# Kernel optimization log

Measured on AMD Instinct MI355X. Metric: run time of the kernel, lower is better.

The kernel has to match this reference:

```python
import jax, jax.numpy as jnp
import numpy as np

N_TOKENS, D_MODEL, D_HIDDEN, TOPK = 4096, 1024, 16384, 64


def setup_inputs() -> dict:
    key = jax.random.key(0)
    k0, k1, k2 = jax.random.split(key, 3)
    x = jax.random.normal(k0, (N_TOKENS, D_MODEL), dtype=jnp.float32)
    # kaiming_uniform_(a=sqrt(5)) -> bound = 1/sqrt(fan_in)
    lim_enc = 1.0 / np.sqrt(D_MODEL)
    W_enc = jax.random.uniform(k1, (D_MODEL, D_HIDDEN), jnp.float32, -lim_enc, lim_enc)
    b_enc = jnp.zeros((D_HIDDEN,), jnp.float32)
    lim_dec = 1.0 / np.sqrt(D_HIDDEN)
    W_dec = jax.random.uniform(k2, (D_HIDDEN, D_MODEL), jnp.float32, -lim_dec, lim_dec)
    # normalize_decoder=True: rows (one per feature) are unit-normalized in-place
    # under no_grad in torch, so we pre-normalize the parameter here.
    W_dec = W_dec / jnp.clip(jnp.linalg.norm(W_dec, axis=1, keepdims=True), 1e-8, None)
    b_dec = jnp.zeros((D_MODEL,), jnp.float32)
    return {"x": x, "W_enc": W_enc, "b_enc": b_enc, "W_dec": W_dec, "b_dec": b_dec, "k": TOPK}


def reference(x, W_enc, b_enc, W_dec, b_dec, k):
    # encode
    pre = x @ W_enc + b_enc                     # [N, d_hidden]
    # ReLU activation (config in ('relu','topk'))
    z = jax.nn.relu(pre)
    # TopK on |z| along feature dim, scatter original values back
    _, idx = jax.lax.top_k(jnp.abs(z), k)        # [N, k]
    rows = jnp.arange(z.shape[0])[:, None]       # [N, 1]
    z_sparse = jnp.zeros_like(z).at[rows, idx].set(jnp.take_along_axis(z, idx, axis=-1))
    # decode (W_dec rows are already unit-norm; torch re-normalizes under no_grad)
    y = z_sparse @ W_dec + b_dec                # [N, d_model]
    return y
```

## Files before the change

kernel.cpp:

```cpp
#include <hip/hip_runtime.h>

typedef unsigned short ushort_t;
typedef unsigned short ushort8 __attribute__((ext_vector_type(8)));
typedef __bf16 bf16x8 __attribute__((ext_vector_type(8)));
typedef float f32x4 __attribute__((ext_vector_type(4)));

#define N_TOKENS 4096
#define D_MODEL  1024
#define D_HIDDEN 16384
#define TOPK     64
#define DELTA    0.03f
#define RCAP     128
#define T0SEL    1.25f
#define CAP      512

__device__ __forceinline__ float bf2f(ushort_t u) {
  union { unsigned u; float f; } c; c.u = ((unsigned)u) << 16; return c.f;
}
__device__ __forceinline__ ushort_t f2bf(float f) {
  union { float f; unsigned u; } c; c.f = f;
  unsigned x = c.u;
  unsigned r = (x + 0x7FFFu + ((x >> 16) & 1u)) >> 16;
  return (ushort_t)r;
}

typedef __attribute__((address_space(1))) void GV;
typedef __attribute__((address_space(3))) void LV;
__device__ __forceinline__ void llds16(const void* g, void* l) {
  __builtin_amdgcn_global_load_lds((GV*)g, (LV*)l, 16, 0, 0);
}

__global__ __launch_bounds__(256) void cast_x_kernel(
    const float* __restrict__ in, ushort_t* __restrict__ out) {
  const int i = (blockIdx.x * 256 + threadIdx.x) * 4;
  float4 v = *(const float4*)&in[i];
  ushort4 o;
  o.x = f2bf(v.x); o.y = f2bf(v.y); o.z = f2bf(v.z); o.w = f2bf(v.w);
  *(ushort4*)&out[i] = o;
}

__global__ __launch_bounds__(256) void cast_wdec_kernel(
    const float* __restrict__ in, ushort_t* __restrict__ out) {
  const int i = (blockIdx.x * 256 + threadIdx.x) * 8;
  float4 v0 = *(const float4*)&in[i];
  float4 v1 = *(const float4*)&in[i + 4];
  ushort8 o;
  o[0] = f2bf(v0.x); o[1] = f2bf(v0.y); o[2] = f2bf(v0.z); o[3] = f2bf(v0.w);
  o[4] = f2bf(v1.x); o[5] = f2bf(v1.y); o[6] = f2bf(v1.z); o[7] = f2bf(v1.w);
  *(ushort8*)&out[i] = o;
}

__global__ __launch_bounds__(256) void transpose_cast_kernel(
    const float* __restrict__ in, ushort_t* __restrict__ outb,
    float* __restrict__ out32) {
  __shared__ float tile[64][68];
  const int tid = threadIdx.x;
  const int n0 = blockIdx.x * 64;
  const int k0 = blockIdx.y * 64;
#pragma unroll
  for (int i = 0; i < 4; ++i) {
    int e = i * 256 + tid;
    int kk = e >> 4;
    int nn = (e & 15) * 4;
    float4 v = *(const float4*)&in[(size_t)(k0 + kk) * D_HIDDEN + n0 + nn];
    tile[kk][nn + 0] = v.x;
    tile[kk][nn + 1] = v.y;
    tile[kk][nn + 2] = v.z;
    tile[kk][nn + 3] = v.w;
  }
  __syncthreads();
#pragma unroll
  for (int i = 0; i < 4; ++i) {
    int e = i * 256 + tid;
    int nn = e >> 4;
    int kk = (e & 15) * 4;
    float4 f;
    f.x = tile[kk + 0][nn];
    f.y = tile[kk + 1][nn];
    f.z = tile[kk + 2][nn];
    f.w = tile[kk + 3][nn];
    *(float4*)&out32[(size_t)(n0 + nn) * D_MODEL + k0 + kk] = f;
    ushort4 b;
    b.x = f2bf(f.x); b.y = f2bf(f.y); b.z = f2bf(f.z); b.w = f2bf(f.w);
    *(ushort4*)&outb[(size_t)(n0 + nn) * D_MODEL + k0 + kk] = b;
  }
}

__global__ __launch_bounds__(256) void encode_gemm(
    const ushort_t* __restrict__ X, const ushort_t* __restrict__ WT,
    const float* __restrict__ benc, ushort_t* __restrict__ Z) {
  __shared__ ushort_t As[128 * 32];
  __shared__ ushort_t Bs[128 * 32];
  const int tid  = threadIdx.x;
  const int wave = tid >> 6, lane = tid & 63;
  const int m0 = blockIdx.y * 128;
  const int n0 = blockIdx.x * 128;
  const int wm = (wave >> 1) * 64;
  const int wn = (wave & 1) * 64;
  const int lr = lane >> 2;
  const int lk = (lane & 3) * 8;

  f32x4 acc[4][4];
#pragma unroll
  for (int i = 0; i < 4; ++i)
#pragma unroll
    for (int j = 0; j < 4; ++j) acc[i][j] = (f32x4){0.f, 0.f, 0.f, 0.f};

  for (int k0 = 0; k0 < D_MODEL; k0 += 32) {
    __syncthreads();
#pragma unroll
    for (int c = 0; c < 2; ++c) {
      const int chunk = c * 4 + wave;
      const int m = chunk * 16 + lr;
      llds16(&X [(size_t)(m0 + m) * D_MODEL + k0 + lk], &As[chunk * 512]);
      llds16(&WT[(size_t)(n0 + m) * D_MODEL + k0 + lk], &Bs[chunk * 512]);
    }
    __syncthreads();
    bf16x8 af[4], bfr[4];
#pragma unroll
    for (int t = 0; t < 4; ++t) {
      af[t]  = *(const bf16x8*)&As[(wm + t * 16 + (lane & 15)) * 32 + (lane >> 4) * 8];
      bfr[t] = *(const bf16x8*)&Bs[(wn + t * 16 + (lane & 15)) * 32 + (lane >> 4) * 8];
    }
#pragma unroll
    for (int mt = 0; mt < 4; ++mt)
#pragma unroll
      for (int nt = 0; nt < 4; ++nt)
        acc[mt][nt] = __builtin_amdgcn_mfma_f32_16x16x32_bf16(
            af[mt], bfr[nt], acc[mt][nt], 0, 0, 0);
  }

  const int col_base = n0 + wn + (lane & 15);
  const int row_base = m0 + wm + (lane >> 4) * 4;
#pragma unroll
  for (int nt = 0; nt < 4; ++nt) {
    const float bias = benc[col_base + nt * 16];
#pragma unroll
    for (int mt = 0; mt < 4; ++mt) {
#pragma unroll
      for (int r = 0; r < 4; ++r) {
        float v = fmaxf(acc[mt][nt][r] + bias, 0.0f);
        Z[(size_t)(row_base + mt * 16 + r) * D_HIDDEN + col_base + nt * 16] = f2bf(v);
      }
    }
  }
}

__global__ __launch_bounds__(256) void topk_fused_kernel(
    const ushort_t* __restrict__ Z, const float* __restrict__ x32,
    const float* __restrict__ WT32, const float* __restrict__ benc,
    float* __restrict__ vals, int* __restrict__ idxs, int* __restrict__ flags) {
  __shared__ float  sval[CAP];
  __shared__ int    sidx[CAP];
  __shared__ int    wsum[4];
  __shared__ int    ridx[RCAP];
  __shared__ double rex[RCAP];
  __shared__ float  sV64;
  __shared__ int    selCount, refCount;
  const int tid  = threadIdx.x;
  const int lane = tid & 63;
  const int wv   = tid >> 6;
  const int row  = blockIdx.x;
  const ushort_t* zr = Z + (size_t)row * D_HIDDEN;

  ushort8 u8v[8];
#pragma unroll
  for (int i = 0; i < 8; ++i) u8v[i] = *(const ushort8*)&zr[i * 2048 + tid * 8];

  if (tid == 0) { selCount = 0; refCount = 0; }

  int cntT = 0;
#pragma unroll
  for (int i = 0; i < 8; ++i)
#pragma unroll
    for (int j = 0; j < 8; ++j) cntT += (bf2f(u8v[i][j]) > T0SEL) ? 1 : 0;

  int inc = cntT;
#pragma unroll
  for (int off = 1; off < 64; off <<= 1) {
    int y = __shfl_up(inc, off, 64);
    if (lane >= off) inc += y;
  }
  const int excT = inc - cntT;
  if (lane == 63) wsum[wv] = inc;
  __syncthreads();
  int base = excT;
  if (wv > 0) base += wsum[0];
  if (wv > 1) base += wsum[1];
  if (wv > 2) base += wsum[2];
  const int n = wsum[0] + wsum[1] + wsum[2] + wsum[3];

  int p = base;
#pragma unroll
  for (int i = 0; i < 8; ++i)
#pragma unroll
    for (int j = 0; j < 8; ++j) {
      const float f = bf2f(u8v[i][j]);
      if (f > T0SEL) {
        if (p < CAP) { sval[p] = f; sidx[p] = i * 2048 + tid * 8 + j; }
        ++p;
      }
    }
  __syncthreads();
  if (n < TOPK || n > CAP) { if (tid == 0) flags[row] = 1; return; }

  for (int j = tid; j < n; j += 256) {
    float vj = sval[j]; int ij = sidx[j];
    int rank = 0;
    for (int j2 = 0; j2 < n; ++j2) {
      float v2 = sval[j2];
      rank += (v2 > vj) || (v2 == vj && sidx[j2] < ij);
    }
    if (rank == TOPK - 1) sV64 = vj;
  }
  __syncthreads();
  const float v64 = sV64;
  if (v64 <= T0SEL + DELTA) { if (tid == 0) flags[row] = 1; return; }

  for (int j = tid; j < n; j += 256) {
    float v = sval[j];
    if (v > v64 + DELTA) {
      int p2 = atomicAdd(&selCount, 1);
      vals[(size_t)row * TOPK + p2] = v;
      idxs[(size_t)row * TOPK + p2] = sidx[j];
    } else if (v >= v64 - DELTA) {
      int c = atomicAdd(&refCount, 1);
      if (c < RCAP) ridx[c] = sidx[j];
    }
  }
  __syncthreads();
  if (refCount > RCAP) { if (tid == 0) flags[row] = 1; return; }
  if (tid == 0) flags[row] = 0;
  const int nS = selCount;
  const int nR = refCount;
  const int rNeed = TOPK - nS;

  float xr[16];
  {
    const float* xrb = &x32[(size_t)row * D_MODEL + lane * 16];
#pragma unroll
    for (int q = 0; q < 4; ++q)
      *(float4*)&xr[q * 4] = *(const float4*)&xrb[q * 4];
  }
  for (int c = wv; c < nR; c += 4) {
    const int j = ridx[c];
    const float* wr = &WT32[(size_t)j * D_MODEL];
    double p0 = 0.0, p1 = 0.0;
#pragma unroll
    for (int q = 0; q < 2; ++q) {
      const float4 wa = *(const float4*)&wr[lane * 16 + q * 8];
      const float4 wb = *(const float4*)&wr[lane * 16 + q * 8 + 4];
      p0 += (double)xr[q * 8 + 0] * wa.x + (double)xr[q * 8 + 1] * wa.y
          + (double)xr[q * 8 + 2] * wa.z + (double)xr[q * 8 + 3] * wa.w;
      p1 += (double)xr[q * 8 + 4] * wb.x + (double)xr[q * 8 + 5] * wb.y
          + (double)xr[q * 8 + 6] * wb.z + (double)xr[q * 8 + 7] * wb.w;
    }
    double part = p0 + p1;
#pragma unroll
    for (int off = 32; off > 0; off >>= 1) part += __shfl_down(part, off, 64);
    if (lane == 0) {
      double d = part + (double)benc[j];
      rex[c] = d > 0.0 ? d : 0.0;
    }
  }
  __syncthreads();

  for (int c = tid; c < nR; c += 256) {
    double vc = rex[c]; int ic = ridx[c];
    int rank = 0;
    for (int c2 = 0; c2 < nR; ++c2) {
      double v2 = rex[c2];
      rank += (v2 > vc) || (v2 == vc && ridx[c2] < ic);
    }
    if (rank < rNeed) {
      int p2 = atomicAdd(&selCount, 1);
      vals[(size_t)row * TOPK + p2] = (float)vc;
      idxs[(size_t)row * TOPK + p2] = ic;
    }
  }
}

__global__ __launch_bounds__(256) void topk_fallback_kernel(
    const int* __restrict__ flags,
    const ushort_t* __restrict__ Z, const float* __restrict__ x32,
    const float* __restrict__ WT32, const float* __restrict__ benc,
    float* __restrict__ vals, int* __restrict__ idxs) {
  if (flags[blockIdx.x] == 0) return;
  __shared__ int hist[512 * 9 + 32];
  float*  cval = (float*)hist;
  int*    cidx = (int*)hist + 512;
  int*    ridx = (int*)hist + 1024;
  double* rex  = (double*)((int*)hist + 1156);
  __shared__ int   wtot[4];
  __shared__ int   sTbin, sAbove, selCount, candCount, refCount;
  __shared__ float sV64;

  const int tid  = threadIdx.x;
  const int wave = tid >> 6, lane = tid & 63;
  const int row  = blockIdx.x;
  const ushort_t* zr = Z + (size_t)row * D_HIDDEN;

  ushort8 u8v[8];
#pragma unroll
  for (int i = 0; i < 8; ++i) u8v[i] = *(const ushort8*)&zr[i * 2048 + tid * 8];
#define ZIDX(i, j) ((i) * 2048 + tid * 8 + (j))

  for (int k = tid; k < 512 * 9; k += 256) hist[k] = 0;
  if (tid == 0) { sTbin = -1; selCount = 0; candCount = 0; refCount = 0; }
  __syncthreads();

  const int cpy = lane & 7;
#pragma unroll
  for (int i = 0; i < 8; ++i)
#pragma unroll
    for (int j = 0; j < 8; ++j) {
      ushort_t w = u8v[i][j];
      if (w) atomicAdd(&hist[((int)(w >> 6)) * 9 + cpy], 1);
    }
  __syncthreads();

  int h0 = 0, h1 = 0;
#pragma unroll
  for (int c = 0; c < 8; ++c) {
    int cc = (tid + c) & 7;
    h0 += hist[(2 * tid) * 9 + cc];
    h1 += hist[(2 * tid + 1) * 9 + cc];
  }
  const int s = h0 + h1;
  int x = s;
#pragma unroll
  for (int off = 1; off < 64; off <<= 1) {
    int y = __shfl_down(x, off, 64);
    if (lane + off < 64) x += y;
  }
  if (lane == 0) wtot[wave] = x;
  __syncthreads();
  int cross = 0;
  if (wave < 3) cross += wtot[3];
  if (wave < 2) cross += wtot[2];
  if (wave < 1) cross += wtot[1];
  const int Sexc = cross + x - s;
  if (Sexc < TOPK && Sexc + h1 >= TOPK) { sTbin = 2 * tid + 1; sAbove = Sexc; }
  const int c0 = Sexc + h1;
  if (c0 < TOPK && c0 + h0 >= TOPK) { sTbin = 2 * tid; sAbove = c0; }
  __syncthreads();
  const int Tbin = sTbin, nAbove = sAbove;

  if (Tbin < 0) {
#pragma unroll
    for (int i = 0; i < 8; ++i)
#pragma unroll
      for (int j = 0; j < 8; ++j) {
        ushort_t w = u8v[i][j];
        if (w) {
          int p = atomicAdd(&selCount, 1);
          if (p < TOPK) { vals[row * 64 + p] = bf2f(w); idxs[row * 64 + p] = ZIDX(i, j); }
        }
      }
    __syncthreads();
    for (int p2 = min(selCount, TOPK) + tid; p2 < TOPK; p2 += 256) {
      vals[row * 64 + p2] = 0.0f; idxs[row * 64 + p2] = 0;
    }
    return;
  }

#pragma unroll
  for (int i = 0; i < 8; ++i)
#pragma unroll
    for (int j = 0; j < 8; ++j) {
      ushort_t w = u8v[i][j];
      if (w && (int)(w >> 6) == Tbin) {
        int c = atomicAdd(&candCount, 1);
        if (c < 512) { cval[c] = bf2f(w); cidx[c] = ZIDX(i, j); }
      }
    }
  __syncthreads();
  {
    const int r  = TOPK - nAbove;
    const int nc = min(candCount, 512);
    for (int j = tid; j < nc; j += 256) {
      float vj = cval[j]; int ij = cidx[j];
      int rank = 0;
      for (int j2 = 0; j2 < nc; ++j2) {
        float v2 = cval[j2];
        rank += (v2 > vj) || (v2 == vj && cidx[j2] < ij);
      }
      if (rank == r - 1) sV64 = vj;
    }
  }
  __syncthreads();
  const float v64 = sV64;

#pragma unroll
  for (int i = 0; i < 8; ++i)
#pragma unroll
    for (int j = 0; j < 8; ++j) {
      ushort_t w = u8v[i][j];
      if (!w) continue;
      float v = bf2f(w);
      if (v > v64 + DELTA) {
        int p = atomicAdd(&selCount, 1);
        vals[row * 64 + p] = v;
        idxs[row * 64 + p] = ZIDX(i, j);
      } else if (v >= v64 - DELTA) {
        int c = atomicAdd(&refCount, 1);
        if (c < RCAP) ridx[c] = ZIDX(i, j);
      }
    }
  __syncthreads();
  const int nS = selCount;
  const int nR = min(refCount, RCAP);
  const int rNeed = TOPK - nS;

  float xr[16];
  {
    const float* xrb = &x32[(size_t)row * D_MODEL + lane * 16];
#pragma unroll
    for (int q = 0; q < 4; ++q)
      *(float4*)&xr[q * 4] = *(const float4*)&xrb[q * 4];
  }
  for (int c = wave; c < nR; c += 4) {
    const int j = ridx[c];
    const float* wr = &WT32[(size_t)j * D_MODEL];
    double p0 = 0.0, p1 = 0.0;
#pragma unroll
    for (int q = 0; q < 2; ++q) {
      const float4 wa = *(const float4*)&wr[lane * 16 + q * 8];
      const float4 wb = *(const float4*)&wr[lane * 16 + q * 8 + 4];
      p0 += (double)xr[q * 8 + 0] * wa.x + (double)xr[q * 8 + 1] * wa.y
          + (double)xr[q * 8 + 2] * wa.z + (double)xr[q * 8 + 3] * wa.w;
      p1 += (double)xr[q * 8 + 4] * wb.x + (double)xr[q * 8 + 5] * wb.y
          + (double)xr[q * 8 + 6] * wb.z + (double)xr[q * 8 + 7] * wb.w;
    }
    double part = p0 + p1;
#pragma unroll
    for (int off = 32; off > 0; off >>= 1) part += __shfl_down(part, off, 64);
    if (lane == 0) {
      double d = part + (double)benc[j];
      rex[c] = d > 0.0 ? d : 0.0;
    }
  }
  __syncthreads();

  for (int c = tid; c < nR; c += 256) {
    double vc = rex[c]; int ic = ridx[c];
    int rank = 0;
    for (int c2 = 0; c2 < nR; ++c2) {
      double v2 = rex[c2];
      rank += (v2 > vc) || (v2 == vc && ridx[c2] < ic);
    }
    if (rank < rNeed) {
      int p = atomicAdd(&selCount, 1);
      vals[row * 64 + p] = (float)vc;
      idxs[row * 64 + p] = ic;
    }
  }
}

__global__ __launch_bounds__(256) void decode_kernel(
    const float* __restrict__ vals, const int* __restrict__ idxs,
    const ushort_t* __restrict__ Wdec_bf, const float* __restrict__ bdec,
    float* __restrict__ Y) {
  __shared__ float sv[2][TOPK];
  __shared__ int   si[2][TOPK];
  const int tid = threadIdx.x;
  const int r0  = blockIdx.x * 2;
  if (tid < 128) {
    int rr = tid >> 6, jj = tid & 63;
    sv[rr][jj] = vals[(r0 + rr) * 64 + jj];
    si[rr][jj] = idxs[(r0 + rr) * 64 + jj];
  }
  __syncthreads();
  const int rr  = tid >> 7;
  const int c0  = (tid & 127) * 8;
  const int row = r0 + rr;
  float4 b0 = *(const float4*)&bdec[c0];
  float4 b1 = *(const float4*)&bdec[c0 + 4];
  float a[8] = {b0.x, b0.y, b0.z, b0.w, b1.x, b1.y, b1.z, b1.w};
#pragma unroll 8
  for (int j = 0; j < TOPK; ++j) {
    const float vj = sv[rr][j];
    ushort8 w = *(const ushort8*)&Wdec_bf[(size_t)si[rr][j] * D_MODEL + c0];
#pragma unroll
    for (int u = 0; u < 8; ++u) a[u] += vj * bf2f(w[u]);
  }
  *(float4*)&Y[(size_t)row * D_MODEL + c0]     = (float4){a[0], a[1], a[2], a[3]};
  *(float4*)&Y[(size_t)row * D_MODEL + c0 + 4] = (float4){a[4], a[5], a[6], a[7]};
}

extern "C" void kernel_launch(void* const* d_in, const int* in_sizes, int n_in,
                              void* d_out, int out_size, void* d_ws, size_t ws_size,
                              hipStream_t stream) {
  const float* x     = (const float*)d_in[0];
  const float* W_enc = (const float*)d_in[1];
  const float* b_enc = (const float*)d_in[2];
  const float* W_dec = (const float*)d_in[3];
  const float* b_dec = (const float*)d_in[4];

  const size_t WT_BYTES   = (size_t)D_HIDDEN * D_MODEL * sizeof(ushort_t);
  const size_t WT32_BYTES = (size_t)D_HIDDEN * D_MODEL * sizeof(float);
  const size_t XB_BYTES   = (size_t)N_TOKENS * D_MODEL * sizeof(ushort_t);
  const size_t V_BYTES    = (size_t)N_TOKENS * TOPK * sizeof(float);
  const size_t F_BYTES    = (size_t)N_TOKENS * sizeof(int);
  const size_t FIXED      = WT_BYTES + WT32_BYTES + XB_BYTES + 2 * V_BYTES
                          + F_BYTES;

  int chunk_rows = 4096;
  while (chunk_rows > 128 &&
         FIXED + (size_t)chunk_rows * D_HIDDEN * sizeof(ushort_t) > ws_size)
    chunk_rows >>= 1;

  char* ws = (char*)d_ws;
  size_t off = 0;
  ushort_t* WT    = (ushort_t*)(ws + off); off += WT_BYTES;
  float*    WT32  = (float*)(ws + off);    off += WT32_BYTES;
  ushort_t* XB    = (ushort_t*)(ws + off); off += XB_BYTES;
  float*    vals  = (float*)(ws + off);    off += V_BYTES;
  int*      idxs  = (int*)(ws + off);      off += V_BYTES;
  int*      flags = (int*)(ws + off);      off += F_BYTES;
  ushort_t* Z     = (ushort_t*)(ws + off);
  float*    Y     = (float*)d_out;

  cast_x_kernel<<<dim3(N_TOKENS * D_MODEL / 1024), 256, 0, stream>>>(x, XB);
  transpose_cast_kernel<<<dim3(D_HIDDEN / 64, D_MODEL / 64), 256, 0, stream>>>(
      W_enc, WT, WT32);

  for (int r0 = 0; r0 < N_TOKENS; r0 += chunk_rows) {
    encode_gemm<<<dim3(D_HIDDEN / 128, chunk_rows / 128), 256, 0, stream>>>(
        XB + (size_t)r0 * D_MODEL, WT, b_enc, Z);
    topk_fused_kernel<<<dim3(chunk_rows), 256, 0, stream>>>(
        Z, x + (size_t)r0 * D_MODEL, WT32, b_enc,
        vals + (size_t)r0 * TOPK, idxs + (size_t)r0 * TOPK, flags + r0);
    topk_fallback_kernel<<<dim3(chunk_rows), 256, 0, stream>>>(
        flags + r0, Z, x + (size_t)r0 * D_MODEL, WT32, b_enc,
        vals + (size_t)r0 * TOPK, idxs + (size_t)r0 * TOPK);
  }

  cast_wdec_kernel<<<dim3(D_HIDDEN * D_MODEL / (256 * 8)), 256, 0, stream>>>(W_dec, WT);

  decode_kernel<<<dim3(N_TOKENS / 2), 256, 0, stream>>>(vals, idxs, WT, b_dec, Y);
}
```

Baseline: 620.9 us.

## Emit per-tile threshold candidates from encode GEMM epilogue to skip Z rescan

The encode GEMM epilogue now collects, per output row and 128-column tile, the activations above the selection threshold into LDS slots (up to 15), packed as bf16 value plus column. These are written to a compact candidate buffer. The top-k select kernel reads that buffer instead of rereading the full bf16 Z row, which cuts its global traffic. The cost is LDS atomics and extra stores in the GEMM epilogue, plus a new fallback trigger whenever any tile overflows its slots. Z is still written for the fallback path.

Result: slower. 669.1 us (+7.8%).

```diff
diff --git a/kernel.cpp b/kernel.cpp
--- a/kernel.cpp
+++ b/kernel.cpp
@@ -4,6 +4,7 @@
 typedef unsigned short ushort8 __attribute__((ext_vector_type(8)));
 typedef __bf16 bf16x8 __attribute__((ext_vector_type(8)));
 typedef float f32x4 __attribute__((ext_vector_type(4)));
+typedef unsigned int uint_t;
 
 #define N_TOKENS 4096
 #define D_MODEL  1024
@@ -13,6 +14,7 @@
 #define RCAP     128
 #define T0SEL    1.25f
 #define CAP      512
+#define SSL      15
 
 __device__ __forceinline__ float bf2f(ushort_t u) {
   union { unsigned u; float f; } c; c.u = ((unsigned)u) << 16; return c.f;
@@ -88,7 +90,8 @@
 
 __global__ __launch_bounds__(256) void encode_gemm(
     const ushort_t* __restrict__ X, const ushort_t* __restrict__ WT,
-    const float* __restrict__ benc, ushort_t* __restrict__ Z) {
+    const float* __restrict__ benc, ushort_t* __restrict__ Z,
+    uint_t* __restrict__ cand) {
   __shared__ ushort_t As[128 * 32];
   __shared__ ushort_t Bs[128 * 32];
   const int tid  = threadIdx.x;
@@ -130,8 +133,16 @@
             af[mt], bfr[nt], acc[mt][nt], 0, 0, 0);
   }
 
-  const int col_base = n0 + wn + (lane & 15);
-  const int row_base = m0 + wm + (lane >> 4) * 4;
+  uint_t* slots = (uint_t*)As;
+  int*    lcnt  = (int*)Bs;
+  __syncthreads();
+  if (tid < 128) lcnt[tid] = 0;
+  __syncthreads();
+
+  const int col_base  = n0 + wn + (lane & 15);
+  const int lcol_base = wn + (lane & 15);
+  const int row_base  = m0 + wm + (lane >> 4) * 4;
+  const int lrow_base = wm + (lane >> 4) * 4;
 #pragma unroll
   for (int nt = 0; nt < 4; ++nt) {
     const float bias = benc[col_base + nt * 16];
@@ -141,68 +152,94 @@
       for (int r = 0; r < 4; ++r) {
         float v = fmaxf(acc[mt][nt][r] + bias, 0.0f);
         Z[(size_t)(row_base + mt * 16 + r) * D_HIDDEN + col_base + nt * 16] = f2bf(v);
+        if (v > T0SEL) {
+          const int lrw = lrow_base + mt * 16 + r;
+          int p = atomicAdd(&lcnt[lrw], 1);
+          if (p < SSL)
+            slots[lrw * SSL + p] =
+                ((uint_t)f2bf(v) << 16) | (uint_t)(lcol_base + nt * 16);
+        }
       }
     }
   }
-}
-
-__global__ __launch_bounds__(256) void topk_fused_kernel(
-    const ushort_t* __restrict__ Z, const float* __restrict__ x32,
+  __syncthreads();
+
+  if (tid < 128) {
+    const int c = lcnt[tid];
+    const uint_t* s = &slots[tid * SSL];
+    uint4 w0 = {s[0],  s[1],  s[2],  s[3]};
+    uint4 w1 = {s[4],  s[5],  s[6],  s[7]};
+    uint4 w2 = {s[8],  s[9],  s[10], s[11]};
+    uint4 w3 = {s[12], s[13], s[14], (uint_t)c};
+    uint_t* dst = cand + ((size_t)(m0 + tid) * 128 + blockIdx.x) * 16;
+    ((uint4*)dst)[0] = w0;
+    ((uint4*)dst)[1] = w1;
+    ((uint4*)dst)[2] = w2;
+    ((uint4*)dst)[3] = w3;
+  }
+}
+
+__global__ __launch_bounds__(256) void topk_select_kernel(
+    const uint_t* __restrict__ cand, const float* __restrict__ x32,
     const float* __restrict__ WT32, const float* __restrict__ benc,
     float* __restrict__ vals, int* __restrict__ idxs, int* __restrict__ flags) {
   __shared__ float  sval[CAP];
   __shared__ int    sidx[CAP];
-  __shared__ int    wsum[4];
+  __shared__ int    wsum[2];
   __shared__ int    ridx[RCAP];
   __shared__ double rex[RCAP];
   __shared__ float  sV64;
-  __shared__ int    selCount, refCount;
+  __shared__ int    selCount, refCount, sOver;
   const int tid  = threadIdx.x;
   const int lane = tid & 63;
   const int wv   = tid >> 6;
   const int row  = blockIdx.x;
-  const ushort_t* zr = Z + (size_t)row * D_HIDDEN;
-
-  ushort8 u8v[8];
-#pragma unroll
-  for (int i = 0; i < 8; ++i) u8v[i] = *(const ushort8*)&zr[i * 2048 + tid * 8];
-
-  if (tid == 0) { selCount = 0; refCount = 0; }
-
-  int cntT = 0;
-#pragma unroll
-  for (int i = 0; i < 8; ++i)
-#pragma unroll
-    for (int j = 0; j < 8; ++j) cntT += (bf2f(u8v[i][j]) > T0SEL) ? 1 : 0;
-
-  int inc = cntT;
+
+  uint4 e0, e1, e2, e3;
+  if (tid < 128) {
+    const uint_t* seg = cand + ((size_t)row * 128 + tid) * 16;
+    e0 = ((const uint4*)seg)[0];
+    e1 = ((const uint4*)seg)[1];
+    e2 = ((const uint4*)seg)[2];
+    e3 = ((const uint4*)seg)[3];
+  }
+  if (tid == 0) { selCount = 0; refCount = 0; sOver = 0; }
+  __syncthreads();
+
+  int myc = 0;
+  if (tid < 128) {
+    myc = (int)e3.w;
+    if (myc > SSL) sOver = 1;
+  }
+  const int valid = (tid < 128) ? min(myc, SSL) : 0;
+
+  int inc = valid;
 #pragma unroll
   for (int off = 1; off < 64; off <<= 1) {
     int y = __shfl_up(inc, off, 64);
     if (lane >= off) inc += y;
   }
-  const int excT = inc - cntT;
-  if (lane == 63) wsum[wv] = inc;
-  __syncthreads();
-  int base = excT;
-  if (wv > 0) base += wsum[0];
-  if (wv > 1) base += wsum[1];
-  if (wv > 2) base += wsum[2];
-  const int n = wsum[0] + wsum[1] + wsum[2] + wsum[3];
-
-  int p = base;
-#pragma unroll
-  for (int i = 0; i < 8; ++i)
-#pragma unroll
-    for (int j = 0; j < 8; ++j) {
-      const float f = bf2f(u8v[i][j]);
-      if (f > T0SEL) {
-        if (p < CAP) { sval[p] = f; sidx[p] = i * 2048 + tid * 8 + j; }
-        ++p;
-      }
-    }
-  __syncthreads();
-  if (n < TOPK || n > CAP) { if (tid == 0) flags[row] = 1; return; }
+  if (lane == 63 && wv < 2) wsum[wv] = inc;
+  __syncthreads();
+  const int base = inc - valid + ((wv == 1) ? wsum[0] : 0);
+  const int n = wsum[0] + wsum[1];
+  if (sOver || n < TOPK || n > CAP) { if (tid == 0) flags[row] = 1; return; }
+
+#define EMIT(k, pv)                                                       \
+  if ((k) < valid) {                                                      \
+    const uint_t p = (pv);                                                \
+    const int q = base + (k);                                             \
+    sval[q] = bf2f((ushort_t)(p >> 16));                                  \
+    sidx[q] = (tid << 7) | (int)(p & 0x7Fu);                              \
+  }
+  if (tid < 128) {
+    EMIT(0, e0.x)  EMIT(1, e0.y)  EMIT(2, e0.z)  EMIT(3, e0.w)
+    EMIT(4, e1.x)  EMIT(5, e1.y)  EMIT(6, e1.z)  EMIT(7, e1.w)
+    EMIT(8, e2.x)  EMIT(9, e2.y)  EMIT(10, e2.z) EMIT(11, e2.w)
+    EMIT(12, e3.x) EMIT(13, e3.y) EMIT(14, e3.z)
+  }
+#undef EMIT
+  __syncthreads();
 
   for (int j = tid; j < n; j += 256) {
     float vj = sval[j]; int ij = sidx[j];
@@ -502,8 +539,9 @@
   const size_t XB_BYTES   = (size_t)N_TOKENS * D_MODEL * sizeof(ushort_t);
   const size_t V_BYTES    = (size_t)N_TOKENS * TOPK * sizeof(float);
   const size_t F_BYTES    = (size_t)N_TOKENS * sizeof(int);
+  const size_t CAND_BYTES = (size_t)N_TOKENS * 128 * 64;
   const size_t FIXED      = WT_BYTES + WT32_BYTES + XB_BYTES + 2 * V_BYTES
-                          + F_BYTES;
+                          + F_BYTES + CAND_BYTES;
 
   int chunk_rows = 4096;
   while (chunk_rows > 128 &&
@@ -518,6 +556,7 @@
   float*    vals  = (float*)(ws + off);    off += V_BYTES;
   int*      idxs  = (int*)(ws + off);      off += V_BYTES;
   int*      flags = (int*)(ws + off);      off += F_BYTES;
+  uint_t*   cand  = (uint_t*)(ws + off);   off += CAND_BYTES;
   ushort_t* Z     = (ushort_t*)(ws + off);
   float*    Y     = (float*)d_out;
 
@@ -527,9 +566,9 @@
 
   for (int r0 = 0; r0 < N_TOKENS; r0 += chunk_rows) {
     encode_gemm<<<dim3(D_HIDDEN / 128, chunk_rows / 128), 256, 0, stream>>>(
-        XB + (size_t)r0 * D_MODEL, WT, b_enc, Z);
-    topk_fused_kernel<<<dim3(chunk_rows), 256, 0, stream>>>(
-        Z, x + (size_t)r0 * D_MODEL, WT32, b_enc,
+        XB + (size_t)r0 * D_MODEL, WT, b_enc, Z, cand + (size_t)r0 * 128 * 16);
+    topk_select_kernel<<<dim3(chunk_rows), 256, 0, stream>>>(
+        cand + (size_t)r0 * 128 * 16, x + (size_t)r0 * D_MODEL, WT32, b_enc,
         vals + (size_t)r0 * TOPK, idxs + (size_t)r0 * TOPK, flags + r0);
     topk_fallback_kernel<<<dim3(chunk_rows), 256, 0, stream>>>(
         flags + r0, Z, x + (size_t)r0 * D_MODEL, WT32, b_enc,
```
